# Kernel optimization log

Measured on AMD Instinct MI355X. Metric: run time of the kernel, lower is better.

The kernel has to match this reference:

```python
import jax, jax.numpy as jnp
import numpy as np

N_NODES = 500_000
N_EDGES = 1_000_000
N_GRAPHS = 5_000
NUM_SHAPES = 16
NUM_COLORS = 16
NUM_REL = 3
NUM_CLASS = 10


def setup_inputs() -> dict:
    key = jax.random.key(0)
    ks = jax.random.split(key, 16)
    s = 0.1
    inp = {
        "x": jax.random.randint(ks[0], (N_NODES, 2), 0, NUM_SHAPES, dtype=jnp.int32),
        "edge_index": jax.random.randint(ks[1], (2, N_EDGES), 0, N_NODES, dtype=jnp.int32),
        "edge_type": jax.random.randint(ks[2], (N_EDGES,), 0, NUM_REL, dtype=jnp.int32),
        "ptr": jnp.arange(0, N_NODES + 1, N_NODES // N_GRAPHS, dtype=jnp.int32),  # [G+1]
        "shape_emb": jax.random.normal(ks[3], (NUM_SHAPES, 8), jnp.float32) * s,
        "color_emb": jax.random.normal(ks[4], (NUM_COLORS, 8), jnp.float32) * s,
        "pre_w": jax.random.normal(ks[5], (16, 32), jnp.float32) * s,
        "pre_b": jnp.zeros((32,), jnp.float32),
        "w1_rel": jax.random.normal(ks[6], (NUM_REL, 32, 64), jnp.float32) * s,
        "w1_root": jax.random.normal(ks[7], (32, 64), jnp.float32) * s,
        "b1": jnp.zeros((64,), jnp.float32),
        "w2_rel": jax.random.normal(ks[8], (NUM_REL, 64, 64), jnp.float32) * s,
        "w2_root": jax.random.normal(ks[9], (64, 64), jnp.float32) * s,
        "b2": jnp.zeros((64,), jnp.float32),
        "cls_w": jax.random.normal(ks[10], (64, NUM_CLASS), jnp.float32) * s,
        "cls_b": jnp.zeros((NUM_CLASS,), jnp.float32),
    }
    return inp


def rgcn_layer(h, w_rel, w_root, b, src, dst, etype):
    # PyG RGCNConv: out_i = bias + x_i @ root + sum_r mean_{j in N_r(i)} x_j @ W_r
    n = h.shape[0]
    hr = jnp.einsum('ni,rio->rno', h, w_rel)          # [R, N, F_out]: per-relation transform
    msg = hr[etype, src]                              # [E, F_out]: gather per-edge message
    seg = etype * n + dst                             # relation-separated segment ids
    agg = jax.ops.segment_sum(msg, seg, num_segments=NUM_REL * n)
    cnt = jax.ops.segment_sum(jnp.ones((msg.shape[0],), h.dtype), seg, num_segments=NUM_REL * n)
    agg = (agg / jnp.maximum(cnt, 1.0)[:, None]).reshape(NUM_REL, n, -1).sum(0)
    return agg + h @ w_root + b


def reference(x, edge_index, edge_type, ptr, shape_emb, color_emb, pre_w, pre_b,
              w1_rel, w1_root, b1, w2_rel, w2_root, b2, cls_w, cls_b):
    src, dst = edge_index[0], edge_index[1]
    h = jnp.concatenate([shape_emb[x[:, 0]], color_emb[x[:, 1]]], axis=1)  # [N,16]
    h = jax.nn.relu(h @ pre_w + pre_b)                                     # [N,32]
    h = jax.nn.relu(rgcn_layer(h, w1_rel, w1_root, b1, src, dst, edge_type))
    h = jax.nn.relu(rgcn_layer(h, w2_rel, w2_root, b2, src, dst, edge_type))
    last_idx = ptr[1:] - 1                                                 # [G]
    return h[last_idx] @ cls_w + cls_b                                     # [G, num_class]
```

## Files before the change

kernel.cpp:

```cpp
#include <hip/hip_runtime.h>

#define NB     64
#define CS     16
#define CAP1   32768
#define BC1    (CAP1 / NB)
#define ROWCAP 20
#define PMASK  0xFFFFF
#define CTRB(b) ((b) * CS)

__device__ __forceinline__ int bittest(const unsigned* bm, int n) {
    return (bm[n >> 5] >> (n & 31)) & 1u;
}

__device__ __forceinline__ void claim1(int n, int* __restrict__ slot1,
                                       int* __restrict__ ctr, int bucket,
                                       const int* __restrict__ x,
                                       int* __restrict__ snode) {
    if (atomicCAS(&slot1[n], 0, -1) == 0) {
        int p = atomicAdd(&ctr[CTRB(bucket)], 1);
        if (p < BC1) {
            int sl = bucket * BC1 + p;
            snode[sl] = x[2 * n] | (x[2 * n + 1] << 4);
            atomicExch(&slot1[n], sl + 1);
        }
    }
}

__global__ void scan1_k(const int* __restrict__ src, const int* __restrict__ dst,
                        const int* __restrict__ et, const int* __restrict__ x,
                        int* __restrict__ slot1, int* __restrict__ snode,
                        int* __restrict__ pgE, int* __restrict__ ecnt2,
                        unsigned* __restrict__ bitN1, int* __restrict__ ctr,
                        int nE, int G, unsigned long long M, int stride) {
    int tid = blockIdx.x * blockDim.x + threadIdx.x;
    int nT  = gridDim.x * blockDim.x;
    for (int g = tid; g < G; g += nT) {
        int last = (g + 1) * stride - 1;
        atomicOr(&bitN1[last >> 5], 1u << (last & 31));
        claim1(last, slot1, ctr, g & (NB - 1), x, snode);
    }
    int bucket = (tid >> 6) & (NB - 1);
    int nC = (nE + 3) >> 2;
    for (int c = tid; c < nC; c += nT) {
        int e0 = c * 4;
        int d[4];
        int cnt = min(4, nE - e0);
        if (cnt == 4) { int4 v = *(const int4*)(dst + e0); d[0]=v.x; d[1]=v.y; d[2]=v.z; d[3]=v.w; }
        else for (int k = 0; k < cnt; k++) d[k] = dst[e0 + k];
#pragma unroll
        for (int k = 0; k < 4; k++) {
            if (k >= cnt) break;
            unsigned dk = (unsigned)d[k];
            unsigned q = (unsigned)(((unsigned long long)dk * M) >> 42);
            if ((int)(dk - q * (unsigned)stride) == stride - 1) {
                int e = e0 + k;
                int s = src[e], r = et[e];
                int idx = atomicAdd(&ecnt2[q], 1);
                if (idx < ROWCAP) pgE[q * ROWCAP + idx] = s | (r << 20);
                atomicOr(&bitN1[s >> 5], 1u << (s & 31));
                claim1(s, slot1, ctr, bucket, x, snode);
            }
        }
    }
}

__global__ void scan2_k(const int* __restrict__ src, const int* __restrict__ dst,
                        const int* __restrict__ et, const int* __restrict__ x,
                        const unsigned* __restrict__ bitN1,
                        const int* __restrict__ slot1, int* __restrict__ psE,
                        int* __restrict__ ecnt1, int nE) {
    int tid = blockIdx.x * blockDim.x + threadIdx.x;
    int nT  = gridDim.x * blockDim.x;
    int nC = (nE + 3) >> 2;
    for (int c = tid; c < nC; c += nT) {
        int e0 = c * 4;
        int d[4];
        int cnt = min(4, nE - e0);
        if (cnt == 4) { int4 v = *(const int4*)(dst + e0); d[0]=v.x; d[1]=v.y; d[2]=v.z; d[3]=v.w; }
        else for (int k = 0; k < cnt; k++) d[k] = dst[e0 + k];
#pragma unroll
        for (int k = 0; k < 4; k++) {
            if (k >= cnt) break;
            if (bittest(bitN1, d[k])) {
                int e = e0 + k;
                int s1 = slot1[d[k]] - 1;
                if (s1 >= 0) {
                    int s = src[e];
                    int pk = et[e] | (x[2 * s] << 4) | (x[2 * s + 1] << 8);
                    int idx = atomicAdd(&ecnt1[s1], 1);
                    if (idx < ROWCAP) psE[s1 * ROWCAP + idx] = pk;
                }
            }
        }
    }
}

__device__ __forceinline__ float h0_of(int x0, int x1, int fh, float pbv,
        const float* __restrict__ s_se, const float* __restrict__ s_ce,
        const float* __restrict__ s_pw) {
    float h0 = pbv;
#pragma unroll
    for (int k = 0; k < 8; k++)
        h0 += s_se[x0 * 8 + k] * s_pw[k * 32 + fh] +
              s_ce[x1 * 8 + k] * s_pw[(k + 8) * 32 + fh];
    return fmaxf(h0, 0.f);
}

__device__ __forceinline__ void edge_acc(int pk, int fh, float pbv,
        const float* __restrict__ s_se, const float* __restrict__ s_ce,
        const float* __restrict__ s_pw,
        float& a0, float& a1, float& a2, int& c0, int& c1, int& c2) {
    int r = pk & 15, x0 = (pk >> 4) & 15, x1 = (pk >> 8) & 15;
    float h0 = h0_of(x0, x1, fh, pbv, s_se, s_ce, s_pw);
    if (r == 0)      { a0 += h0; c0++; }
    else if (r == 1) { a1 += h0; c1++; }
    else             { a2 += h0; c2++; }
}

__device__ __forceinline__ float mm32(const float* __restrict__ sa,
                                      const float* __restrict__ w, int f) {
    float s0 = 0.f, s1 = 0.f, s2 = 0.f, s3 = 0.f;
#pragma unroll
    for (int k = 0; k < 32; k += 4) {
        float4 a = *(const float4*)(sa + k);
        s0 += a.x * w[(k + 0) * 64 + f];
        s1 += a.y * w[(k + 1) * 64 + f];
        s2 += a.z * w[(k + 2) * 64 + f];
        s3 += a.w * w[(k + 3) * 64 + f];
    }
    return (s0 + s1) + (s2 + s3);
}

__device__ __forceinline__ float mm64(const float* __restrict__ sa,
                                      const float* __restrict__ w, int f) {
    float s0 = 0.f, s1 = 0.f, s2 = 0.f, s3 = 0.f;
#pragma unroll
    for (int k = 0; k < 64; k += 4) {
        float4 a = *(const float4*)(sa + k);
        s0 += a.x * w[(k + 0) * 64 + f];
        s1 += a.y * w[(k + 1) * 64 + f];
        s2 += a.z * w[(k + 2) * 64 + f];
        s3 += a.w * w[(k + 3) * 64 + f];
    }
    return (s0 + s1) + (s2 + s3);
}

__global__ __launch_bounds__(256, 2) void h1_k(
        const int* __restrict__ snode, const int* __restrict__ psE,
        const int* __restrict__ ecnt1, const int* __restrict__ ctr,
        const float* __restrict__ se, const float* __restrict__ ce,
        const float* __restrict__ pw, const float* __restrict__ pb,
        const float* __restrict__ w1r, const float* __restrict__ wroot1,
        const float* __restrict__ b1, float* __restrict__ h1buf) {
    __shared__ __align__(16) float smem[9472];
    int t = threadIdx.x;
    float4* s4 = (float4*)smem;
    for (int i = t; i < 1536; i += 256) s4[i] = ((const float4*)w1r)[i];
    for (int i = t; i < 512;  i += 256) s4[1536 + i] = ((const float4*)wroot1)[i];
    if (t < 32)       s4[2048 + t] = ((const float4*)se)[t];
    else if (t < 64)  s4[2048 + t] = ((const float4*)ce)[t - 32];
    if (t < 128) s4[2112 + t] = ((const float4*)pw)[t];
    __syncthreads();
    const float* s_w1  = smem;
    const float* s_wr1 = smem + 6144;
    const float* s_se  = smem + 8192;
    const float* s_ce  = smem + 8320;
    const float* s_pw  = smem + 8448;
    float* sv = smem + 8960 + (t >> 6) * 128;
    int lane = t & 63, f = lane, fh = f & 31;
    float bias1 = b1[f];
    float pbv   = pb[fh];
    int wv  = (blockIdx.x << 2) + (t >> 6);
    int nwv = gridDim.x << 2;
    int b   = wv & (NB - 1);
    int nj  = nwv >> 6;
    int cnt = min(ctr[CTRB(b)], BC1);
    int p = wv >> 6;
    if (p >= cnt) return;
    int sl = b * BC1 + p;
    int sx = snode[sl];
    int m  = min(ecnt1[sl], ROWCAP);
    int4 v = *(const int4*)(psE + (size_t)sl * ROWCAP);
    while (true) {
        int pn = p + nj;
        bool more = pn < cnt;
        int sxn = 0, mn = 0; int4 vn = make_int4(0, 0, 0, 0);
        if (more) {
            int sln = b * BC1 + pn;
            sxn = snode[sln];
            mn  = min(ecnt1[sln], ROWCAP);
            vn  = *(const int4*)(psE + (size_t)sln * ROWCAP);
        }
        float a0 = 0.f, a1 = 0.f, a2 = 0.f;
        int c0 = 0, c1 = 0, c2 = 0;
        if (m > 0) {
            edge_acc(v.x, fh, pbv, s_se, s_ce, s_pw, a0, a1, a2, c0, c1, c2);
            if (m > 1) edge_acc(v.y, fh, pbv, s_se, s_ce, s_pw, a0, a1, a2, c0, c1, c2);
            if (m > 2) edge_acc(v.z, fh, pbv, s_se, s_ce, s_pw, a0, a1, a2, c0, c1, c2);
            if (m > 3) edge_acc(v.w, fh, pbv, s_se, s_ce, s_pw, a0, a1, a2, c0, c1, c2);
            for (int e = 4; e < m; e++)
                edge_acc(psE[(size_t)sl * ROWCAP + e], fh, pbv, s_se, s_ce, s_pw,
                         a0, a1, a2, c0, c1, c2);
        }
        float h0n = h0_of(sx & 15, (sx >> 4) & 15, fh, pbv, s_se, s_ce, s_pw);
        if (lane < 32) {
            sv[fh]      = h0n;
            sv[32 + fh] = c0 ? a0 * (1.0f / (float)c0) : 0.f;
        } else {
            sv[64 + fh] = c1 ? a1 * (1.0f / (float)c1) : 0.f;
            sv[96 + fh] = c2 ? a2 * (1.0f / (float)c2) : 0.f;
        }
        float acc = bias1 + mm32(sv, s_wr1, f);
        if (c0) acc += mm32(sv + 32, s_w1, f);
        if (c1) acc += mm32(sv + 64, s_w1 + 2048, f);
        if (c2) acc += mm32(sv + 96, s_w1 + 4096, f);
        h1buf[(size_t)sl * 64 + f] = fmaxf(acc, 0.f);
        if (!more) break;
        p = pn; sl = b * BC1 + p; sx = sxn; m = mn; v = vn;
    }
}

__global__ __launch_bounds__(256, 2) void final_k(
        const int* __restrict__ slot1, const float* __restrict__ h1buf,
        const float* __restrict__ w2r, const float* __restrict__ wroot2,
        const float* __restrict__ b2, const float* __restrict__ cw,
        const float* __restrict__ cb, const int* __restrict__ pgE,
        const int* __restrict__ ecnt2, float* __restrict__ out,
        int G, int stride) {
    __shared__ __align__(16) float smem[18048];
    int t = threadIdx.x;
    float4* s4 = (float4*)smem;
    for (int i = t; i < 3072; i += 256) s4[i] = ((const float4*)w2r)[i];
    for (int i = t; i < 1024; i += 256) s4[3072 + i] = ((const float4*)wroot2)[i];
    if (t < 160) s4[4096 + t] = ((const float4*)cw)[t];
    __syncthreads();
    const float* s_w2  = smem;
    const float* s_wr2 = smem + 12288;
    const float* s_cw  = smem + 16384;
    float* sv = smem + 17024 + (t >> 6) * 256;
    int f = t & 63;
    int fc = (f < 10) ? f : 0;
    float bias2 = b2[f];
    float cbv = (f < 10) ? cb[f] : 0.f;
    int wv  = (blockIdx.x << 2) + (t >> 6);
    int nwv = gridDim.x << 2;
    for (int g = wv; g < G; g += nwv) {
        int last = (g + 1) * stride - 1;
        int sll = slot1[last] - 1;
        int m2 = min(ecnt2[g], ROWCAP);
        float a0 = 0.f, a1 = 0.f, a2 = 0.f;
        int c0 = 0, c1 = 0, c2 = 0;
        if (m2 > 0) {
            int4 v = *(const int4*)(pgE + (size_t)g * ROWCAP);
            int q0 = slot1[v.x & PMASK] - 1;
            int q1 = (m2 > 1) ? slot1[v.y & PMASK] - 1 : -1;
            int q2 = (m2 > 2) ? slot1[v.z & PMASK] - 1 : -1;
            int q3 = (m2 > 3) ? slot1[v.w & PMASK] - 1 : -1;
            float h0v = (q0 >= 0) ? h1buf[(size_t)q0 * 64 + f] : 0.f;
            float h1v = (q1 >= 0) ? h1buf[(size_t)q1 * 64 + f] : 0.f;
            float h2v = (q2 >= 0) ? h1buf[(size_t)q2 * 64 + f] : 0.f;
            float h3v = (q3 >= 0) ? h1buf[(size_t)q3 * 64 + f] : 0.f;
            { int r = v.x >> 20;
              if (r == 0) { a0 += h0v; c0++; } else if (r == 1) { a1 += h0v; c1++; } else { a2 += h0v; c2++; } }
            if (m2 > 1) { int r = v.y >> 20;
              if (r == 0) { a0 += h1v; c0++; } else if (r == 1) { a1 += h1v; c1++; } else { a2 += h1v; c2++; } }
            if (m2 > 2) { int r = v.z >> 20;
              if (r == 0) { a0 += h2v; c0++; } else if (r == 1) { a1 += h2v; c1++; } else { a2 += h2v; c2++; } }
            if (m2 > 3) { int r = v.w >> 20;
              if (r == 0) { a0 += h3v; c0++; } else if (r == 1) { a1 += h3v; c1++; } else { a2 += h3v; c2++; } }
            for (int e = 4; e < m2; e++) {
                int pk = pgE[(size_t)g * ROWCAP + e];
                int ss = slot1[pk & PMASK] - 1;
                float hv = (ss >= 0) ? h1buf[(size_t)ss * 64 + f] : 0.f;
                int r = pk >> 20;
                if (r == 0) { a0 += hv; c0++; } else if (r == 1) { a1 += hv; c1++; } else { a2 += hv; c2++; }
            }
        }
        float hlast = (sll >= 0) ? h1buf[(size_t)sll * 64 + f] : 0.f;
        sv[f]       = hlast;
        sv[64 + f]  = c0 ? a0 * (1.0f / (float)c0) : 0.f;
        sv[128 + f] = c1 ? a1 * (1.0f / (float)c1) : 0.f;
        sv[192 + f] = c2 ? a2 * (1.0f / (float)c2) : 0.f;
        float acc = bias2 + mm64(sv, s_wr2, f);
        if (c0) acc += mm64(sv + 64,  s_w2, f);
        if (c1) acc += mm64(sv + 128, s_w2 + 4096, f);
        if (c2) acc += mm64(sv + 192, s_w2 + 8192, f);
        float h2 = fmaxf(acc, 0.0f);
        sv[f] = h2;
        float o = cbv;
#pragma unroll
        for (int k = 0; k < 64; k += 4) {
            float4 a = *(const float4*)(sv + k);
            o += a.x * s_cw[(k + 0) * 10 + fc] + a.y * s_cw[(k + 1) * 10 + fc]
               + a.z * s_cw[(k + 2) * 10 + fc] + a.w * s_cw[(k + 3) * 10 + fc];
        }
        if (f < 10) out[g * 10 + f] = o;
    }
}

static inline size_t rnd(size_t x) { return (x + 255) & ~(size_t)255; }

extern "C" void kernel_launch(void* const* d_in, const int* in_sizes, int n_in,
                              void* d_out, int out_size, void* d_ws, size_t ws_size,
                              hipStream_t stream) {
    const int*   x    = (const int*)d_in[0];
    const int*   ei   = (const int*)d_in[1];
    const int*   et   = (const int*)d_in[2];
    const float* se   = (const float*)d_in[4];
    const float* ce   = (const float*)d_in[5];
    const float* pw   = (const float*)d_in[6];
    const float* pb   = (const float*)d_in[7];
    const float* w1r  = (const float*)d_in[8];
    const float* w1rt = (const float*)d_in[9];
    const float* b1   = (const float*)d_in[10];
    const float* w2r  = (const float*)d_in[11];
    const float* w2rt = (const float*)d_in[12];
    const float* b2   = (const float*)d_in[13];
    const float* cw   = (const float*)d_in[14];
    const float* cb   = (const float*)d_in[15];
    float* out = (float*)d_out;

    const int nN = in_sizes[0] / 2;
    const int nE = in_sizes[2];
    const int G  = in_sizes[3] - 1;
    const int nBW = (nN + 31) / 32;

    const int* src = ei;
    const int* dst = ei + nE;

    const int stride = nN / G;
    const unsigned long long M =
        ((1ULL << 42) + (unsigned long long)stride - 1) / (unsigned long long)stride;

    char* p = (char*)d_ws;
    size_t off = 0;
    auto take = [&](size_t bytes) { size_t o = off; off += rnd(bytes); return o; };

    int*      ctr   = (int*)     (p + take(NB * CS * sizeof(int)));
    unsigned* bitN1 = (unsigned*)(p + take((size_t)nBW * 4));
    int*      ecnt1 = (int*)     (p + take((size_t)CAP1 * 4));
    int*      ecnt2 = (int*)     (p + take((size_t)G * 4));
    int*      slot1 = (int*)     (p + take((size_t)nN * 4));
    size_t zero_bytes = off;
    int*      snode = (int*)     (p + take((size_t)CAP1 * 4));
    int*      psE   = (int*)     (p + take((size_t)CAP1 * ROWCAP * 4));
    int*      pgE   = (int*)     (p + take((size_t)G * ROWCAP * 4));
    float*    h1buf = (float*)   (p + take((size_t)CAP1 * 64 * 4));

    hipMemsetAsync(p, 0, zero_bytes, stream);

    int nT = (nE + 3) / 4;
    scan1_k<<<(nT + 255) / 256, 256, 0, stream>>>(src, dst, et, x, slot1, snode,
                                                  pgE, ecnt2, bitN1, ctr, nE, G, M, stride);
    scan2_k<<<(nT + 255) / 256, 256, 0, stream>>>(src, dst, et, x, bitN1, slot1,
                                                  psE, ecnt1, nE);
    h1_k<<<1024, 256, 0, stream>>>(snode, psE, ecnt1, ctr, se, ce, pw, pb,
                                   w1r, w1rt, b1, h1buf);
    final_k<<<512, 256, 0, stream>>>(slot1, h1buf, w2r, w2rt, b2, cw, cb,
                                     pgE, ecnt2, out, G, stride);
}
```

Baseline: 162.3 us.

## Fuse memset and four kernels into one cooperative kernel with grid syncs

Replaces the memset plus four separate launches (scan1, scan2, h1, final) with a single cooperative kernel of 512 blocks that zeroes the workspace itself and separates the phases with grid-wide syncs. Weights are staged in shared memory once per block and reused across phases. The aim is to remove launch and inter-kernel gaps. In exchange the scan phases run with fewer threads in grid-stride loops, the larger shared-memory footprint may limit occupancy, and the old multi-kernel path is kept as a fallback if the cooperative launch fails.

```diff
diff --git a/kernel.cpp b/kernel.cpp
--- a/kernel.cpp
+++ b/kernel.cpp
@@ -1,4 +1,7 @@
 #include <hip/hip_runtime.h>
+#include <hip/hip_cooperative_groups.h>
+
+namespace cg = cooperative_groups;
 
 #define NB     64
 #define CS     16
@@ -7,6 +10,19 @@
 #define ROWCAP 20
 #define PMASK  0xFFFFF
 #define CTRB(b) ((b) * CS)
+#define GRID   512
+
+struct Params {
+    const int *src, *dst, *et, *x;
+    int *slot1, *snode, *pgE, *ecnt2, *ctr, *ecnt1, *psE;
+    unsigned *bitN1;
+    const float *se, *ce, *pw, *pb, *w1r, *wroot1, *b1;
+    const float *w2r, *wroot2, *b2, *cw, *cb;
+    float *h1buf, *out;
+    int4 *zbase;
+    int zero_i4, nE, G, stride;
+    unsigned long long M;
+};
 
 __device__ __forceinline__ int bittest(const unsigned* bm, int n) {
     return (bm[n >> 5] >> (n & 31)) & 1u;
@@ -22,6 +38,261 @@
             int sl = bucket * BC1 + p;
             snode[sl] = x[2 * n] | (x[2 * n + 1] << 4);
             atomicExch(&slot1[n], sl + 1);
+        }
+    }
+}
+
+__device__ __forceinline__ float h0_of(int x0, int x1, int fh, float pbv,
+        const float* __restrict__ s_se, const float* __restrict__ s_ce,
+        const float* __restrict__ s_pw) {
+    float h0 = pbv;
+#pragma unroll
+    for (int k = 0; k < 8; k++)
+        h0 += s_se[x0 * 8 + k] * s_pw[k * 32 + fh] +
+              s_ce[x1 * 8 + k] * s_pw[(k + 8) * 32 + fh];
+    return fmaxf(h0, 0.f);
+}
+
+__device__ __forceinline__ void edge_acc(int pk, int fh, float pbv,
+        const float* __restrict__ s_se, const float* __restrict__ s_ce,
+        const float* __restrict__ s_pw,
+        float& a0, float& a1, float& a2, int& c0, int& c1, int& c2) {
+    int r = pk & 15, x0 = (pk >> 4) & 15, x1 = (pk >> 8) & 15;
+    float h0 = h0_of(x0, x1, fh, pbv, s_se, s_ce, s_pw);
+    if (r == 0)      { a0 += h0; c0++; }
+    else if (r == 1) { a1 += h0; c1++; }
+    else             { a2 += h0; c2++; }
+}
+
+__device__ __forceinline__ float mm32(const float* __restrict__ sa,
+                                      const float* __restrict__ w, int f) {
+    float s0 = 0.f, s1 = 0.f, s2 = 0.f, s3 = 0.f;
+#pragma unroll
+    for (int k = 0; k < 32; k += 4) {
+        float4 a = *(const float4*)(sa + k);
+        s0 += a.x * w[(k + 0) * 64 + f];
+        s1 += a.y * w[(k + 1) * 64 + f];
+        s2 += a.z * w[(k + 2) * 64 + f];
+        s3 += a.w * w[(k + 3) * 64 + f];
+    }
+    return (s0 + s1) + (s2 + s3);
+}
+
+__device__ __forceinline__ float mm64(const float* __restrict__ sa,
+                                      const float* __restrict__ w, int f) {
+    float s0 = 0.f, s1 = 0.f, s2 = 0.f, s3 = 0.f;
+#pragma unroll
+    for (int k = 0; k < 64; k += 4) {
+        float4 a = *(const float4*)(sa + k);
+        s0 += a.x * w[(k + 0) * 64 + f];
+        s1 += a.y * w[(k + 1) * 64 + f];
+        s2 += a.z * w[(k + 2) * 64 + f];
+        s3 += a.w * w[(k + 3) * 64 + f];
+    }
+    return (s0 + s1) + (s2 + s3);
+}
+
+__global__ __launch_bounds__(256, 2) void fused_k(Params p) {
+    cg::grid_group grid = cg::this_grid();
+    __shared__ __align__(16) float smem[18048];
+    int t = threadIdx.x;
+    int tid = blockIdx.x * blockDim.x + t;
+    int nT  = gridDim.x * blockDim.x;
+    int lane = t & 63, f = lane, fh = f & 31;
+
+    for (int i = tid; i < p.zero_i4; i += nT) p.zbase[i] = make_int4(0, 0, 0, 0);
+    float4* s4 = (float4*)smem;
+    for (int i = t; i < 1536; i += 256) s4[i] = ((const float4*)p.w1r)[i];
+    for (int i = t; i < 512;  i += 256) s4[1536 + i] = ((const float4*)p.wroot1)[i];
+    if (t < 32)       s4[2048 + t] = ((const float4*)p.se)[t];
+    else if (t < 64)  s4[2048 + t] = ((const float4*)p.ce)[t - 32];
+    if (t < 128) s4[2112 + t] = ((const float4*)p.pw)[t];
+    float bias1 = p.b1[f];
+    float pbv   = p.pb[fh];
+    float bias2 = p.b2[f];
+    float cbv   = (f < 10) ? p.cb[f] : 0.f;
+    grid.sync();
+
+    {
+        for (int g = tid; g < p.G; g += nT) {
+            int last = (g + 1) * p.stride - 1;
+            atomicOr(&p.bitN1[last >> 5], 1u << (last & 31));
+            claim1(last, p.slot1, p.ctr, g & (NB - 1), p.x, p.snode);
+        }
+        int bucket = (tid >> 6) & (NB - 1);
+        int nC = (p.nE + 3) >> 2;
+        for (int c = tid; c < nC; c += nT) {
+            int e0 = c * 4;
+            int d[4];
+            int cnt = min(4, p.nE - e0);
+            if (cnt == 4) { int4 v = *(const int4*)(p.dst + e0); d[0]=v.x; d[1]=v.y; d[2]=v.z; d[3]=v.w; }
+            else for (int k = 0; k < cnt; k++) d[k] = p.dst[e0 + k];
+#pragma unroll
+            for (int k = 0; k < 4; k++) {
+                if (k >= cnt) break;
+                unsigned dk = (unsigned)d[k];
+                unsigned q = (unsigned)(((unsigned long long)dk * p.M) >> 42);
+                if ((int)(dk - q * (unsigned)p.stride) == p.stride - 1) {
+                    int e = e0 + k;
+                    int s = p.src[e], r = p.et[e];
+                    int idx = atomicAdd(&p.ecnt2[q], 1);
+                    if (idx < ROWCAP) p.pgE[q * ROWCAP + idx] = s | (r << 20);
+                    atomicOr(&p.bitN1[s >> 5], 1u << (s & 31));
+                    claim1(s, p.slot1, p.ctr, bucket, p.x, p.snode);
+                }
+            }
+        }
+    }
+    grid.sync();
+
+    {
+        int nC = (p.nE + 3) >> 2;
+        for (int c = tid; c < nC; c += nT) {
+            int e0 = c * 4;
+            int d[4];
+            int cnt = min(4, p.nE - e0);
+            if (cnt == 4) { int4 v = *(const int4*)(p.dst + e0); d[0]=v.x; d[1]=v.y; d[2]=v.z; d[3]=v.w; }
+            else for (int k = 0; k < cnt; k++) d[k] = p.dst[e0 + k];
+#pragma unroll
+            for (int k = 0; k < 4; k++) {
+                if (k >= cnt) break;
+                if (bittest(p.bitN1, d[k])) {
+                    int e = e0 + k;
+                    int s1 = p.slot1[d[k]] - 1;
+                    if (s1 >= 0) {
+                        int s = p.src[e];
+                        int pk = p.et[e] | (p.x[2 * s] << 4) | (p.x[2 * s + 1] << 8);
+                        int idx = atomicAdd(&p.ecnt1[s1], 1);
+                        if (idx < ROWCAP) p.psE[s1 * ROWCAP + idx] = pk;
+                    }
+                }
+            }
+        }
+    }
+    grid.sync();
+
+    {
+        const float* s_w1  = smem;
+        const float* s_wr1 = smem + 6144;
+        const float* s_se  = smem + 8192;
+        const float* s_ce  = smem + 8320;
+        const float* s_pw  = smem + 8448;
+        float* sv = smem + 8960 + (t >> 6) * 128;
+        int wv  = (blockIdx.x << 2) + (t >> 6);
+        int nwv = gridDim.x << 2;
+        int b   = wv & (NB - 1);
+        int nj  = nwv >> 6;
+        int cnt = min(p.ctr[CTRB(b)], BC1);
+        int q = wv >> 6;
+        if (q < cnt) {
+            int sl = b * BC1 + q;
+            int sx = p.snode[sl];
+            int m  = min(p.ecnt1[sl], ROWCAP);
+            int4 v = *(const int4*)(p.psE + (size_t)sl * ROWCAP);
+            while (true) {
+                int qn = q + nj;
+                bool more = qn < cnt;
+                int sxn = 0, mn = 0; int4 vn = make_int4(0, 0, 0, 0);
+                if (more) {
+                    int sln = b * BC1 + qn;
+                    sxn = p.snode[sln];
+                    mn  = min(p.ecnt1[sln], ROWCAP);
+                    vn  = *(const int4*)(p.psE + (size_t)sln * ROWCAP);
+                }
+                float a0 = 0.f, a1 = 0.f, a2 = 0.f;
+                int c0 = 0, c1 = 0, c2 = 0;
+                if (m > 0) {
+                    edge_acc(v.x, fh, pbv, s_se, s_ce, s_pw, a0, a1, a2, c0, c1, c2);
+                    if (m > 1) edge_acc(v.y, fh, pbv, s_se, s_ce, s_pw, a0, a1, a2, c0, c1, c2);
+                    if (m > 2) edge_acc(v.z, fh, pbv, s_se, s_ce, s_pw, a0, a1, a2, c0, c1, c2);
+                    if (m > 3) edge_acc(v.w, fh, pbv, s_se, s_ce, s_pw, a0, a1, a2, c0, c1, c2);
+                    for (int e = 4; e < m; e++)
+                        edge_acc(p.psE[(size_t)sl * ROWCAP + e], fh, pbv, s_se, s_ce, s_pw,
+                                 a0, a1, a2, c0, c1, c2);
+                }
+                float h0n = h0_of(sx & 15, (sx >> 4) & 15, fh, pbv, s_se, s_ce, s_pw);
+                if (lane < 32) {
+                    sv[fh]      = h0n;
+                    sv[32 + fh] = c0 ? a0 * (1.0f / (float)c0) : 0.f;
+                } else {
+                    sv[64 + fh] = c1 ? a1 * (1.0f / (float)c1) : 0.f;
+                    sv[96 + fh] = c2 ? a2 * (1.0f / (float)c2) : 0.f;
+                }
+                float acc = bias1 + mm32(sv, s_wr1, f);
+                if (c0) acc += mm32(sv + 32, s_w1, f);
+                if (c1) acc += mm32(sv + 64, s_w1 + 2048, f);
+                if (c2) acc += mm32(sv + 96, s_w1 + 4096, f);
+                p.h1buf[(size_t)sl * 64 + f] = fmaxf(acc, 0.f);
+                if (!more) break;
+                q = qn; sl = b * BC1 + q; sx = sxn; m = mn; v = vn;
+            }
+        }
+    }
+    grid.sync();
+
+    for (int i = t; i < 3072; i += 256) s4[i] = ((const float4*)p.w2r)[i];
+    for (int i = t; i < 1024; i += 256) s4[3072 + i] = ((const float4*)p.wroot2)[i];
+    if (t < 160) s4[4096 + t] = ((const float4*)p.cw)[t];
+    __syncthreads();
+    {
+        const float* s_w2  = smem;
+        const float* s_wr2 = smem + 12288;
+        const float* s_cw  = smem + 16384;
+        float* sv = smem + 17024 + (t >> 6) * 256;
+        int fc = (f < 10) ? f : 0;
+        int wv  = (blockIdx.x << 2) + (t >> 6);
+        int nwv = gridDim.x << 2;
+        for (int g = wv; g < p.G; g += nwv) {
+            int last = (g + 1) * p.stride - 1;
+            int sll = p.slot1[last] - 1;
+            int m2 = min(p.ecnt2[g], ROWCAP);
+            float a0 = 0.f, a1 = 0.f, a2 = 0.f;
+            int c0 = 0, c1 = 0, c2 = 0;
+            if (m2 > 0) {
+                int4 v = *(const int4*)(p.pgE + (size_t)g * ROWCAP);
+                int q0 = p.slot1[v.x & PMASK] - 1;
+                int q1 = (m2 > 1) ? p.slot1[v.y & PMASK] - 1 : -1;
+                int q2 = (m2 > 2) ? p.slot1[v.z & PMASK] - 1 : -1;
+                int q3 = (m2 > 3) ? p.slot1[v.w & PMASK] - 1 : -1;
+                float h0v = (q0 >= 0) ? p.h1buf[(size_t)q0 * 64 + f] : 0.f;
+                float h1v = (q1 >= 0) ? p.h1buf[(size_t)q1 * 64 + f] : 0.f;
+                float h2v = (q2 >= 0) ? p.h1buf[(size_t)q2 * 64 + f] : 0.f;
+                float h3v = (q3 >= 0) ? p.h1buf[(size_t)q3 * 64 + f] : 0.f;
+                { int r = v.x >> 20;
+                  if (r == 0) { a0 += h0v; c0++; } else if (r == 1) { a1 += h0v; c1++; } else { a2 += h0v; c2++; } }
+                if (m2 > 1) { int r = v.y >> 20;
+                  if (r == 0) { a0 += h1v; c0++; } else if (r == 1) { a1 += h1v; c1++; } else { a2 += h1v; c2++; } }
+                if (m2 > 2) { int r = v.z >> 20;
+                  if (r == 0) { a0 += h2v; c0++; } else if (r == 1) { a1 += h2v; c1++; } else { a2 += h2v; c2++; } }
+                if (m2 > 3) { int r = v.w >> 20;
+                  if (r == 0) { a0 += h3v; c0++; } else if (r == 1) { a1 += h3v; c1++; } else { a2 += h3v; c2++; } }
+                for (int e = 4; e < m2; e++) {
+                    int pk = p.pgE[(size_t)g * ROWCAP + e];
+                    int ss = p.slot1[pk & PMASK] - 1;
+                    float hv = (ss >= 0) ? p.h1buf[(size_t)ss * 64 + f] : 0.f;
+                    int r = pk >> 20;
+                    if (r == 0) { a0 += hv; c0++; } else if (r == 1) { a1 += hv; c1++; } else { a2 += hv; c2++; }
+                }
+            }
+            float hlast = (sll >= 0) ? p.h1buf[(size_t)sll * 64 + f] : 0.f;
+            sv[f]       = hlast;
+            sv[64 + f]  = c0 ? a0 * (1.0f / (float)c0) : 0.f;
+            sv[128 + f] = c1 ? a1 * (1.0f / (float)c1) : 0.f;
+            sv[192 + f] = c2 ? a2 * (1.0f / (float)c2) : 0.f;
+            float acc = bias2 + mm64(sv, s_wr2, f);
+            if (c0) acc += mm64(sv + 64,  s_w2, f);
+            if (c1) acc += mm64(sv + 128, s_w2 + 4096, f);
+            if (c2) acc += mm64(sv + 192, s_w2 + 8192, f);
+            float h2 = fmaxf(acc, 0.0f);
+            sv[f] = h2;
+            float o = cbv;
+#pragma unroll
+            for (int k = 0; k < 64; k += 4) {
+                float4 a = *(const float4*)(sv + k);
+                o += a.x * s_cw[(k + 0) * 10 + fc] + a.y * s_cw[(k + 1) * 10 + fc]
+                   + a.z * s_cw[(k + 2) * 10 + fc] + a.w * s_cw[(k + 3) * 10 + fc];
+            }
+            if (f < 10) p.out[g * 10 + f] = o;
         }
     }
 }
@@ -93,56 +364,6 @@
             }
         }
     }
-}
-
-__device__ __forceinline__ float h0_of(int x0, int x1, int fh, float pbv,
-        const float* __restrict__ s_se, const float* __restrict__ s_ce,
-        const float* __restrict__ s_pw) {
-    float h0 = pbv;
-#pragma unroll
-    for (int k = 0; k < 8; k++)
-        h0 += s_se[x0 * 8 + k] * s_pw[k * 32 + fh] +
-              s_ce[x1 * 8 + k] * s_pw[(k + 8) * 32 + fh];
-    return fmaxf(h0, 0.f);
-}
-
-__device__ __forceinline__ void edge_acc(int pk, int fh, float pbv,
-        const float* __restrict__ s_se, const float* __restrict__ s_ce,
-        const float* __restrict__ s_pw,
-        float& a0, float& a1, float& a2, int& c0, int& c1, int& c2) {
-    int r = pk & 15, x0 = (pk >> 4) & 15, x1 = (pk >> 8) & 15;
-    float h0 = h0_of(x0, x1, fh, pbv, s_se, s_ce, s_pw);
-    if (r == 0)      { a0 += h0; c0++; }
-    else if (r == 1) { a1 += h0; c1++; }
-    else             { a2 += h0; c2++; }
-}
-
-__device__ __forceinline__ float mm32(const float* __restrict__ sa,
-                                      const float* __restrict__ w, int f) {
-    float s0 = 0.f, s1 = 0.f, s2 = 0.f, s3 = 0.f;
-#pragma unroll
-    for (int k = 0; k < 32; k += 4) {
-        float4 a = *(const float4*)(sa + k);
-        s0 += a.x * w[(k + 0) * 64 + f];
-        s1 += a.y * w[(k + 1) * 64 + f];
-        s2 += a.z * w[(k + 2) * 64 + f];
-        s3 += a.w * w[(k + 3) * 64 + f];
-    }
-    return (s0 + s1) + (s2 + s3);
-}
-
-__device__ __forceinline__ float mm64(const float* __restrict__ sa,
-                                      const float* __restrict__ w, int f) {
-    float s0 = 0.f, s1 = 0.f, s2 = 0.f, s3 = 0.f;
-#pragma unroll
-    for (int k = 0; k < 64; k += 4) {
-        float4 a = *(const float4*)(sa + k);
-        s0 += a.x * w[(k + 0) * 64 + f];
-        s1 += a.y * w[(k + 1) * 64 + f];
-        s2 += a.z * w[(k + 2) * 64 + f];
-        s3 += a.w * w[(k + 3) * 64 + f];
-    }
-    return (s0 + s1) + (s2 + s3);
 }
 
 __global__ __launch_bounds__(256, 2) void h1_k(
@@ -347,15 +568,31 @@
     int*      pgE   = (int*)     (p + take((size_t)G * ROWCAP * 4));
     float*    h1buf = (float*)   (p + take((size_t)CAP1 * 64 * 4));
 
-    hipMemsetAsync(p, 0, zero_bytes, stream);
-
-    int nT = (nE + 3) / 4;
-    scan1_k<<<(nT + 255) / 256, 256, 0, stream>>>(src, dst, et, x, slot1, snode,
-                                                  pgE, ecnt2, bitN1, ctr, nE, G, M, stride);
-    scan2_k<<<(nT + 255) / 256, 256, 0, stream>>>(src, dst, et, x, bitN1, slot1,
-                                                  psE, ecnt1, nE);
-    h1_k<<<1024, 256, 0, stream>>>(snode, psE, ecnt1, ctr, se, ce, pw, pb,
-                                   w1r, w1rt, b1, h1buf);
-    final_k<<<512, 256, 0, stream>>>(slot1, h1buf, w2r, w2rt, b2, cw, cb,
-                                     pgE, ecnt2, out, G, stride);
-}
+    Params prm;
+    prm.src = src; prm.dst = dst; prm.et = et; prm.x = x;
+    prm.slot1 = slot1; prm.snode = snode; prm.pgE = pgE; prm.ecnt2 = ecnt2;
+    prm.ctr = ctr; prm.ecnt1 = ecnt1; prm.psE = psE; prm.bitN1 = bitN1;
+    prm.se = se; prm.ce = ce; prm.pw = pw; prm.pb = pb;
+    prm.w1r = w1r; prm.wroot1 = w1rt; prm.b1 = b1;
+    prm.w2r = w2r; prm.wroot2 = w2rt; prm.b2 = b2; prm.cw = cw; prm.cb = cb;
+    prm.h1buf = h1buf; prm.out = out;
+    prm.zbase = (int4*)p; prm.zero_i4 = (int)(zero_bytes / 16);
+    prm.nE = nE; prm.G = G; prm.stride = stride; prm.M = M;
+
+    void* kargs[] = { &prm };
+    hipError_t err = hipLaunchCooperativeKernel((const void*)fused_k, dim3(GRID),
+                                                dim3(256), kargs, 0u, stream);
+    if (err != hipSuccess) {
+        (void)hipGetLastError();
+        hipMemsetAsync(p, 0, zero_bytes, stream);
+        int nT = (nE + 3) / 4;
+        scan1_k<<<(nT + 255) / 256, 256, 0, stream>>>(src, dst, et, x, slot1, snode,
+                                                      pgE, ecnt2, bitN1, ctr, nE, G, M, stride);
+        scan2_k<<<(nT + 255) / 256, 256, 0, stream>>>(src, dst, et, x, bitN1, slot1,
+                                                      psE, ecnt1, nE);
+        h1_k<<<1024, 256, 0, stream>>>(snode, psE, ecnt1, ctr, se, ce, pw, pb,
+                                       w1r, w1rt, b1, h1buf);
+        final_k<<<512, 256, 0, stream>>>(slot1, h1buf, w2r, w2rt, b2, cw, cb,
+                                         pgE, ecnt2, out, G, stride);
+    }
+}
```

After: 401.1 us. 2.47x slower.

## Reserve fixed slots for graph-last nodes and drop bucketed slot counters

Applied to the files above, without the earlier changes.

Graph-last nodes now get slots 0..G-1 directly, so their layer-1 edge lists are written into psE during scan1 and reused from pgE counts. Non-last sources are claimed through a single global counter instead of 64 bucketed counters. final_k resolves last-node rows arithmetically rather than through slot1 lookups, reads wroot2 from global memory to shrink shared memory, and launches more blocks with a higher occupancy hint. The aims are fewer atomics and lookups, a smaller LDS footprint and better occupancy. The cost is contention on one global atomic counter and uncached root-weight reads.

```diff
diff --git a/kernel.cpp b/kernel.cpp
--- a/kernel.cpp
+++ b/kernel.cpp
@@ -1,26 +1,29 @@
 #include <hip/hip_runtime.h>
 
-#define NB     64
-#define CS     16
 #define CAP1   32768
-#define BC1    (CAP1 / NB)
 #define ROWCAP 20
 #define PMASK  0xFFFFF
-#define CTRB(b) ((b) * CS)
 
 __device__ __forceinline__ int bittest(const unsigned* bm, int n) {
     return (bm[n >> 5] >> (n & 31)) & 1u;
 }
 
+__device__ __forceinline__ int is_last(unsigned n, unsigned long long M,
+                                       int stride, unsigned& q) {
+    q = (unsigned)(((unsigned long long)n * M) >> 42);
+    return (int)(n - q * (unsigned)stride) == stride - 1;
+}
+
 __device__ __forceinline__ void claim1(int n, int* __restrict__ slot1,
-                                       int* __restrict__ ctr, int bucket,
+                                       int* __restrict__ ctr,
                                        const int* __restrict__ x,
-                                       int* __restrict__ snode) {
+                                       int* __restrict__ snode, int G) {
     if (atomicCAS(&slot1[n], 0, -1) == 0) {
-        int p = atomicAdd(&ctr[CTRB(bucket)], 1);
-        if (p < BC1) {
-            int sl = bucket * BC1 + p;
-            snode[sl] = x[2 * n] | (x[2 * n + 1] << 4);
+        int p = atomicAdd(ctr, 1);
+        int sl = G + p;
+        if (sl < CAP1) {
+            int2 xv = *(const int2*)(x + 2 * n);
+            snode[sl] = xv.x | (xv.y << 4);
             atomicExch(&slot1[n], sl + 1);
         }
     }
@@ -29,17 +32,17 @@
 __global__ void scan1_k(const int* __restrict__ src, const int* __restrict__ dst,
                         const int* __restrict__ et, const int* __restrict__ x,
                         int* __restrict__ slot1, int* __restrict__ snode,
-                        int* __restrict__ pgE, int* __restrict__ ecnt2,
-                        unsigned* __restrict__ bitN1, int* __restrict__ ctr,
-                        int nE, int G, unsigned long long M, int stride) {
+                        int* __restrict__ pgE, int* __restrict__ psE,
+                        int* __restrict__ ecnt2, unsigned* __restrict__ bitN1,
+                        int* __restrict__ ctr, int nE, int G,
+                        unsigned long long M, int stride) {
     int tid = blockIdx.x * blockDim.x + threadIdx.x;
     int nT  = gridDim.x * blockDim.x;
     for (int g = tid; g < G; g += nT) {
-        int last = (g + 1) * stride - 1;
-        atomicOr(&bitN1[last >> 5], 1u << (last & 31));
-        claim1(last, slot1, ctr, g & (NB - 1), x, snode);
-    }
-    int bucket = (tid >> 6) & (NB - 1);
+        int L = (g + 1) * stride - 1;
+        int2 xv = *(const int2*)(x + 2 * L);
+        snode[g] = xv.x | (xv.y << 4);
+    }
     int nC = (nE + 3) >> 2;
     for (int c = tid; c < nC; c += nT) {
         int e0 = c * 4;
@@ -50,15 +53,21 @@
 #pragma unroll
         for (int k = 0; k < 4; k++) {
             if (k >= cnt) break;
-            unsigned dk = (unsigned)d[k];
-            unsigned q = (unsigned)(((unsigned long long)dk * M) >> 42);
-            if ((int)(dk - q * (unsigned)stride) == stride - 1) {
+            unsigned q;
+            if (is_last((unsigned)d[k], M, stride, q)) {
                 int e = e0 + k;
                 int s = src[e], r = et[e];
                 int idx = atomicAdd(&ecnt2[q], 1);
-                if (idx < ROWCAP) pgE[q * ROWCAP + idx] = s | (r << 20);
-                atomicOr(&bitN1[s >> 5], 1u << (s & 31));
-                claim1(s, slot1, ctr, bucket, x, snode);
+                int2 xv = *(const int2*)(x + 2 * s);
+                if (idx < ROWCAP) {
+                    pgE[q * ROWCAP + idx] = s | (r << 20);
+                    psE[q * ROWCAP + idx] = r | (xv.x << 4) | (xv.y << 8);
+                }
+                unsigned qs;
+                if (!is_last((unsigned)s, M, stride, qs)) {
+                    atomicOr(&bitN1[s >> 5], 1u << (s & 31));
+                    claim1(s, slot1, ctr, x, snode, G);
+                }
             }
         }
     }
@@ -86,7 +95,8 @@
                 int s1 = slot1[d[k]] - 1;
                 if (s1 >= 0) {
                     int s = src[e];
-                    int pk = et[e] | (x[2 * s] << 4) | (x[2 * s + 1] << 8);
+                    int2 xv = *(const int2*)(x + 2 * s);
+                    int pk = et[e] | (xv.x << 4) | (xv.y << 8);
                     int idx = atomicAdd(&ecnt1[s1], 1);
                     if (idx < ROWCAP) psE[s1 * ROWCAP + idx] = pk;
                 }
@@ -147,11 +157,12 @@
 
 __global__ __launch_bounds__(256, 2) void h1_k(
         const int* __restrict__ snode, const int* __restrict__ psE,
-        const int* __restrict__ ecnt1, const int* __restrict__ ctr,
+        const int* __restrict__ ecnt1, const int* __restrict__ ecnt2,
+        const int* __restrict__ ctr,
         const float* __restrict__ se, const float* __restrict__ ce,
         const float* __restrict__ pw, const float* __restrict__ pb,
         const float* __restrict__ w1r, const float* __restrict__ wroot1,
-        const float* __restrict__ b1, float* __restrict__ h1buf) {
+        const float* __restrict__ b1, float* __restrict__ h1buf, int G) {
     __shared__ __align__(16) float smem[9472];
     int t = threadIdx.x;
     float4* s4 = (float4*)smem;
@@ -172,24 +183,20 @@
     float pbv   = pb[fh];
     int wv  = (blockIdx.x << 2) + (t >> 6);
     int nwv = gridDim.x << 2;
-    int b   = wv & (NB - 1);
-    int nj  = nwv >> 6;
-    int cnt = min(ctr[CTRB(b)], BC1);
-    int p = wv >> 6;
-    if (p >= cnt) return;
-    int sl = b * BC1 + p;
-    int sx = snode[sl];
-    int m  = min(ecnt1[sl], ROWCAP);
-    int4 v = *(const int4*)(psE + (size_t)sl * ROWCAP);
+    int nsl = min(G + ctr[0], CAP1);
+    int p = wv;
+    if (p >= nsl) return;
+    int sx = snode[p];
+    int m  = min(p < G ? ecnt2[p] : ecnt1[p], ROWCAP);
+    int4 v = *(const int4*)(psE + (size_t)p * ROWCAP);
     while (true) {
-        int pn = p + nj;
-        bool more = pn < cnt;
+        int pn = p + nwv;
+        bool more = pn < nsl;
         int sxn = 0, mn = 0; int4 vn = make_int4(0, 0, 0, 0);
         if (more) {
-            int sln = b * BC1 + pn;
-            sxn = snode[sln];
-            mn  = min(ecnt1[sln], ROWCAP);
-            vn  = *(const int4*)(psE + (size_t)sln * ROWCAP);
+            sxn = snode[pn];
+            mn  = min(pn < G ? ecnt2[pn] : ecnt1[pn], ROWCAP);
+            vn  = *(const int4*)(psE + (size_t)pn * ROWCAP);
         }
         float a0 = 0.f, a1 = 0.f, a2 = 0.f;
         int c0 = 0, c1 = 0, c2 = 0;
@@ -199,7 +206,7 @@
             if (m > 2) edge_acc(v.z, fh, pbv, s_se, s_ce, s_pw, a0, a1, a2, c0, c1, c2);
             if (m > 3) edge_acc(v.w, fh, pbv, s_se, s_ce, s_pw, a0, a1, a2, c0, c1, c2);
             for (int e = 4; e < m; e++)
-                edge_acc(psE[(size_t)sl * ROWCAP + e], fh, pbv, s_se, s_ce, s_pw,
+                edge_acc(psE[(size_t)p * ROWCAP + e], fh, pbv, s_se, s_ce, s_pw,
                          a0, a1, a2, c0, c1, c2);
         }
         float h0n = h0_of(sx & 15, (sx >> 4) & 15, fh, pbv, s_se, s_ce, s_pw);
@@ -214,30 +221,28 @@
         if (c0) acc += mm32(sv + 32, s_w1, f);
         if (c1) acc += mm32(sv + 64, s_w1 + 2048, f);
         if (c2) acc += mm32(sv + 96, s_w1 + 4096, f);
-        h1buf[(size_t)sl * 64 + f] = fmaxf(acc, 0.f);
+        h1buf[(size_t)p * 64 + f] = fmaxf(acc, 0.f);
         if (!more) break;
-        p = pn; sl = b * BC1 + p; sx = sxn; m = mn; v = vn;
-    }
-}
-
-__global__ __launch_bounds__(256, 2) void final_k(
+        p = pn; sx = sxn; m = mn; v = vn;
+    }
+}
+
+__global__ __launch_bounds__(256, 3) void final_k(
         const int* __restrict__ slot1, const float* __restrict__ h1buf,
         const float* __restrict__ w2r, const float* __restrict__ wroot2,
         const float* __restrict__ b2, const float* __restrict__ cw,
         const float* __restrict__ cb, const int* __restrict__ pgE,
         const int* __restrict__ ecnt2, float* __restrict__ out,
-        int G, int stride) {
-    __shared__ __align__(16) float smem[18048];
+        int G, int stride, unsigned long long M) {
+    __shared__ __align__(16) float smem[13184];
     int t = threadIdx.x;
     float4* s4 = (float4*)smem;
     for (int i = t; i < 3072; i += 256) s4[i] = ((const float4*)w2r)[i];
-    for (int i = t; i < 1024; i += 256) s4[3072 + i] = ((const float4*)wroot2)[i];
-    if (t < 160) s4[4096 + t] = ((const float4*)cw)[t];
+    if (t < 160) s4[3072 + t] = ((const float4*)cw)[t];
     __syncthreads();
-    const float* s_w2  = smem;
-    const float* s_wr2 = smem + 12288;
-    const float* s_cw  = smem + 16384;
-    float* sv = smem + 17024 + (t >> 6) * 256;
+    const float* s_w2 = smem;
+    const float* s_cw = smem + 12288;
+    float* sv = smem + 12928 + (t >> 6) * 64;
     int f = t & 63;
     int fc = (f < 10) ? f : 0;
     float bias2 = b2[f];
@@ -245,46 +250,50 @@
     int wv  = (blockIdx.x << 2) + (t >> 6);
     int nwv = gridDim.x << 2;
     for (int g = wv; g < G; g += nwv) {
-        int last = (g + 1) * stride - 1;
-        int sll = slot1[last] - 1;
         int m2 = min(ecnt2[g], ROWCAP);
         float a0 = 0.f, a1 = 0.f, a2 = 0.f;
         int c0 = 0, c1 = 0, c2 = 0;
         if (m2 > 0) {
             int4 v = *(const int4*)(pgE + (size_t)g * ROWCAP);
-            int q0 = slot1[v.x & PMASK] - 1;
-            int q1 = (m2 > 1) ? slot1[v.y & PMASK] - 1 : -1;
-            int q2 = (m2 > 2) ? slot1[v.z & PMASK] - 1 : -1;
-            int q3 = (m2 > 3) ? slot1[v.w & PMASK] - 1 : -1;
-            float h0v = (q0 >= 0) ? h1buf[(size_t)q0 * 64 + f] : 0.f;
-            float h1v = (q1 >= 0) ? h1buf[(size_t)q1 * 64 + f] : 0.f;
-            float h2v = (q2 >= 0) ? h1buf[(size_t)q2 * 64 + f] : 0.f;
-            float h3v = (q3 >= 0) ? h1buf[(size_t)q3 * 64 + f] : 0.f;
-            { int r = v.x >> 20;
-              if (r == 0) { a0 += h0v; c0++; } else if (r == 1) { a1 += h0v; c1++; } else { a2 += h0v; c2++; } }
-            if (m2 > 1) { int r = v.y >> 20;
-              if (r == 0) { a0 += h1v; c0++; } else if (r == 1) { a1 += h1v; c1++; } else { a2 += h1v; c2++; } }
-            if (m2 > 2) { int r = v.z >> 20;
-              if (r == 0) { a0 += h2v; c0++; } else if (r == 1) { a1 += h2v; c1++; } else { a2 += h2v; c2++; } }
-            if (m2 > 3) { int r = v.w >> 20;
-              if (r == 0) { a0 += h3v; c0++; } else if (r == 1) { a1 += h3v; c1++; } else { a2 += h3v; c2++; } }
+            int row[4]; int rr[4];
+#pragma unroll
+            for (int j = 0; j < 4; j++) {
+                int pk = (j == 0) ? v.x : (j == 1) ? v.y : (j == 2) ? v.z : v.w;
+                int s = pk & PMASK;
+                rr[j] = pk >> 20;
+                unsigned qs;
+                if (j < m2) row[j] = is_last((unsigned)s, M, stride, qs)
+                                       ? (int)qs : slot1[s] - 1;
+                else row[j] = -1;
+            }
+            float hv0 = (row[0] >= 0) ? h1buf[(size_t)row[0] * 64 + f] : 0.f;
+            float hv1 = (row[1] >= 0) ? h1buf[(size_t)row[1] * 64 + f] : 0.f;
+            float hv2 = (row[2] >= 0) ? h1buf[(size_t)row[2] * 64 + f] : 0.f;
+            float hv3 = (row[3] >= 0) ? h1buf[(size_t)row[3] * 64 + f] : 0.f;
+            { int r = rr[0];
+              if (r == 0) { a0 += hv0; c0++; } else if (r == 1) { a1 += hv0; c1++; } else { a2 += hv0; c2++; } }
+            if (m2 > 1) { int r = rr[1];
+              if (r == 0) { a0 += hv1; c0++; } else if (r == 1) { a1 += hv1; c1++; } else { a2 += hv1; c2++; } }
+            if (m2 > 2) { int r = rr[2];
+              if (r == 0) { a0 += hv2; c0++; } else if (r == 1) { a1 += hv2; c1++; } else { a2 += hv2; c2++; } }
+            if (m2 > 3) { int r = rr[3];
+              if (r == 0) { a0 += hv3; c0++; } else if (r == 1) { a1 += hv3; c1++; } else { a2 += hv3; c2++; } }
             for (int e = 4; e < m2; e++) {
                 int pk = pgE[(size_t)g * ROWCAP + e];
-                int ss = slot1[pk & PMASK] - 1;
+                int s = pk & PMASK;
+                unsigned qs;
+                int ss = is_last((unsigned)s, M, stride, qs) ? (int)qs : slot1[s] - 1;
                 float hv = (ss >= 0) ? h1buf[(size_t)ss * 64 + f] : 0.f;
                 int r = pk >> 20;
                 if (r == 0) { a0 += hv; c0++; } else if (r == 1) { a1 += hv; c1++; } else { a2 += hv; c2++; }
             }
         }
-        float hlast = (sll >= 0) ? h1buf[(size_t)sll * 64 + f] : 0.f;
-        sv[f]       = hlast;
-        sv[64 + f]  = c0 ? a0 * (1.0f / (float)c0) : 0.f;
-        sv[128 + f] = c1 ? a1 * (1.0f / (float)c1) : 0.f;
-        sv[192 + f] = c2 ? a2 * (1.0f / (float)c2) : 0.f;
-        float acc = bias2 + mm64(sv, s_wr2, f);
-        if (c0) acc += mm64(sv + 64,  s_w2, f);
-        if (c1) acc += mm64(sv + 128, s_w2 + 4096, f);
-        if (c2) acc += mm64(sv + 192, s_w2 + 8192, f);
+        float hlast = h1buf[(size_t)g * 64 + f];
+        sv[f] = hlast;
+        float acc = bias2 + mm64(sv, wroot2, f);
+        if (c0) { sv[f] = a0 * (1.0f / (float)c0); acc += mm64(sv, s_w2, f); }
+        if (c1) { sv[f] = a1 * (1.0f / (float)c1); acc += mm64(sv, s_w2 + 4096, f); }
+        if (c2) { sv[f] = a2 * (1.0f / (float)c2); acc += mm64(sv, s_w2 + 8192, f); }
         float h2 = fmaxf(acc, 0.0f);
         sv[f] = h2;
         float o = cbv;
@@ -336,7 +345,7 @@
     size_t off = 0;
     auto take = [&](size_t bytes) { size_t o = off; off += rnd(bytes); return o; };
 
-    int*      ctr   = (int*)     (p + take(NB * CS * sizeof(int)));
+    int*      ctr   = (int*)     (p + take(256));
     unsigned* bitN1 = (unsigned*)(p + take((size_t)nBW * 4));
     int*      ecnt1 = (int*)     (p + take((size_t)CAP1 * 4));
     int*      ecnt2 = (int*)     (p + take((size_t)G * 4));
@@ -351,11 +360,12 @@
 
     int nT = (nE + 3) / 4;
     scan1_k<<<(nT + 255) / 256, 256, 0, stream>>>(src, dst, et, x, slot1, snode,
-                                                  pgE, ecnt2, bitN1, ctr, nE, G, M, stride);
+                                                  pgE, psE, ecnt2, bitN1, ctr,
+                                                  nE, G, M, stride);
     scan2_k<<<(nT + 255) / 256, 256, 0, stream>>>(src, dst, et, x, bitN1, slot1,
                                                   psE, ecnt1, nE);
-    h1_k<<<1024, 256, 0, stream>>>(snode, psE, ecnt1, ctr, se, ce, pw, pb,
-                                   w1r, w1rt, b1, h1buf);
-    final_k<<<512, 256, 0, stream>>>(slot1, h1buf, w2r, w2rt, b2, cw, cb,
-                                     pgE, ecnt2, out, G, stride);
-}
+    h1_k<<<1024, 256, 0, stream>>>(snode, psE, ecnt1, ecnt2, ctr, se, ce, pw, pb,
+                                   w1r, w1rt, b1, h1buf, G);
+    final_k<<<768, 256, 0, stream>>>(slot1, h1buf, w2r, w2rt, b2, cw, cb,
+                                     pgE, ecnt2, out, G, stride, M);
+}
```

New measurement: 232.9 us. 43.5% more time.
